# Kernel optimization log

Measured on AMD Instinct MI355X. Metric: run time of the kernel, lower is better.

The kernel has to match this reference:

```python
import jax, jax.numpy as jnp
import numpy as np

OUT_F, IN_F = 8192, 8192
RATIO = 0.05


def setup_inputs() -> dict:
    rng = np.random.default_rng(0)
    # Simulate the quantization performed in OrthoLinear.__init__ with numpy.
    w = (rng.standard_normal((OUT_F, IN_F)) * 0.02).astype(np.float32)
    w_abs = np.abs(w)
    k_idx = min(int(IN_F * 0.995), IN_F - 1)
    # torch.kthvalue(k) = k-th smallest (1-indexed) -> partition index k-1
    robust_max = np.partition(w_abs, k_idx - 1, axis=1)[:, k_idx - 1][:, None]
    robust_max = np.maximum(robust_max, 1e-6)
    scales = (robust_max / 7.0).astype(np.float32)
    w_int = np.clip(np.round(w / scales), -7, 7).astype(np.float32)
    resid = w - w_int * scales
    # top-k |residual| entries form the sparse CSR correction
    k = max(int(resid.size * RATIO), 1)
    metric = np.abs(resid).ravel()
    idx = np.argpartition(metric, -k)[-k:]
    idx.sort()
    rows = idx // IN_F
    cols = (idx % IN_F).astype(np.int32)
    vals = resid.ravel()[idx].astype(np.float16)
    ptr = np.zeros(OUT_F + 1, np.int32)
    ptr[1:] = np.cumsum(np.bincount(rows, minlength=OUT_F)).astype(np.int32)
    # pack two int4 (offset by +8) per byte: even cols -> low nibble, odd -> high
    offs = (w_int + 8.0).astype(np.uint8)
    packed = (offs[:, 0::2] | (offs[:, 1::2] << 4)).astype(np.int32)
    x = jax.random.normal(jax.random.key(0), (4, 8, IN_F), jnp.float32)
    return {
        "x": x,
        "base_packed": jnp.asarray(packed),
        "scales": jnp.asarray(scales.reshape(-1)),
        "ortho_vals": jnp.asarray(vals),
        "ortho_indices": jnp.asarray(cols),
        "ortho_ptr": jnp.asarray(ptr),
        "alpha": jnp.float32(1.0),
    }


def reference(x, base_packed, scales, ortho_vals, ortho_indices, ortho_ptr, alpha):
    lead = x.shape[:-1]
    in_f = x.shape[-1]
    out_f = base_packed.shape[0]
    xf = x.reshape(-1, in_f).astype(jnp.float32)  # [N, in]
    # dequantize packed int4 base weight: interleave low/high nibbles
    low = base_packed & 0xF
    high = (base_packed >> 4) & 0xF
    w_int = jnp.stack([low, high], axis=-1).reshape(out_f, in_f).astype(jnp.float32) - 8.0
    w_base = w_int * scales[:, None]  # [out, in]
    # CSR residual -> scatter into dense [out, in] (disjoint coords), then GEMM
    nnz = ortho_vals.shape[0]
    row_ids = jnp.searchsorted(ortho_ptr, jnp.arange(nnz, dtype=jnp.int32), side="right") - 1
    w_res = jnp.zeros((out_f, in_f), jnp.float32).at[row_ids, ortho_indices].add(
        ortho_vals.astype(jnp.float32)
    )
    out = xf @ w_base.T + alpha * (xf @ w_res.T)  # [N, out]
    return out.reshape(lead + (out_f,))
```

## Files before the change

kernel.cpp:

```cpp
#include <hip/hip_runtime.h>


#define IN_F 8192
#define OUT_F 8192
#define NROW 32
#define KSPLIT 8
#define KSEG (IN_F / KSPLIT)
#define CHUNKS (KSEG / 32)
#define SLICE (NROW * OUT_F)

typedef __attribute__((ext_vector_type(8))) short short8v;
typedef __attribute__((ext_vector_type(4))) float f32x4;

union Frag {
  int4 v;
  unsigned int u[4];
  short8v s;
};

__device__ __forceinline__ unsigned int cvt_pk_bf16(float lo, float hi) {
  unsigned int r;
  asm("v_cvt_pk_bf16_f32 %0, %1, %2" : "=v"(r) : "v"(lo), "v"(hi));
  return r;
}

__device__ __forceinline__ unsigned short f2bf(float f) {
  unsigned int u = __float_as_uint(f);
  u += 0x7FFFu + ((u >> 16) & 1u);
  return (unsigned short)(u >> 16);
}

__global__ __launch_bounds__(256) void prep_kernel(
    const float* __restrict__ x, unsigned short* __restrict__ x_hi,
    unsigned short* __restrict__ x_lo, unsigned short* __restrict__ xTb) {
  __shared__ unsigned short T[64 * 33];
  int tid = threadIdx.x;
  int k0 = blockIdx.x * 64;
  int kk = tid & 63;
  int ng = tid >> 6;
#pragma unroll
  for (int p = 0; p < 8; ++p) {
    int n = p * 4 + ng;
    int idx = n * IN_F + k0 + kk;
    float v = x[idx];
    unsigned short h = f2bf(v);
    float hf = __uint_as_float((unsigned int)h << 16);
    unsigned short l = f2bf(v - hf);
    x_hi[idx] = h;
    x_lo[idx] = l;
    T[kk * 33 + n] = h;
  }
  __syncthreads();
  int kr = tid >> 2, q = tid & 3;
  unsigned int s0 = T[kr * 33 + q * 8 + 0], s1 = T[kr * 33 + q * 8 + 1];
  unsigned int s2 = T[kr * 33 + q * 8 + 2], s3 = T[kr * 33 + q * 8 + 3];
  unsigned int s4 = T[kr * 33 + q * 8 + 4], s5 = T[kr * 33 + q * 8 + 5];
  unsigned int s6 = T[kr * 33 + q * 8 + 6], s7 = T[kr * 33 + q * 8 + 7];
  int4 wv;
  wv.x = (int)(s0 | (s1 << 16));
  wv.y = (int)(s2 | (s3 << 16));
  wv.z = (int)(s4 | (s5 << 16));
  wv.w = (int)(s6 | (s7 << 16));
  ((int4*)xTb)[(size_t)(k0 + kr) * 4 + q] = wv;
}

__global__ __launch_bounds__(256, 4) void dense_kernel(
    const int* __restrict__ packed, const float* __restrict__ scales,
    const unsigned short* __restrict__ x_hi,
    const unsigned short* __restrict__ x_lo, float* __restrict__ part) {
  int tid = threadIdx.x;
  int lane = tid & 63;
  int w = tid >> 6;
  int og = blockIdx.x >> 3;
  int g = blockIdx.x & 7;
  int lo16 = lane & 15;
  int lhi = lane >> 4;

  int o = og * 64 + w * 16 + lo16;
  int kbeg = g * KSEG;
  const int4* wp = (const int4*)(packed + (size_t)o * (IN_F / 2) + (kbeg >> 1)) + lhi;
  const unsigned short* xh = x_hi + lo16 * IN_F + kbeg + 8 * lhi;
  const unsigned short* xl = x_lo + lo16 * IN_F + kbeg + 8 * lhi;

  f32x4 acc0 = {0.f, 0.f, 0.f, 0.f};
  f32x4 acc1 = {0.f, 0.f, 0.f, 0.f};

  Frag wA, h0A, l0A, h1A, l1A;
  Frag wB, h0B, l0B, h1B, l1B;

#define LOADIN(W_, H0, L0, H1, L1, c)                  \
  W_.v = wp[(c) * 4];                                  \
  H0.v = *(const int4*)(xh + (c) * 32);                \
  L0.v = *(const int4*)(xl + (c) * 32);                \
  H1.v = *(const int4*)(xh + 16 * IN_F + (c) * 32);    \
  L1.v = *(const int4*)(xl + 16 * IN_F + (c) * 32);

#define COMPUTE(W_, H0, L0, H1, L1)                                               \
  {                                                                               \
    Frag b;                                                                       \
    b.u[0] = cvt_pk_bf16((float)(W_.v.x & 15) - 8.0f, (float)(W_.v.x >> 4) - 8.0f); \
    b.u[1] = cvt_pk_bf16((float)(W_.v.y & 15) - 8.0f, (float)(W_.v.y >> 4) - 8.0f); \
    b.u[2] = cvt_pk_bf16((float)(W_.v.z & 15) - 8.0f, (float)(W_.v.z >> 4) - 8.0f); \
    b.u[3] = cvt_pk_bf16((float)(W_.v.w & 15) - 8.0f, (float)(W_.v.w >> 4) - 8.0f); \
    acc0 = __builtin_amdgcn_mfma_f32_16x16x32_bf16(H0.s, b.s, acc0, 0, 0, 0);     \
    acc0 = __builtin_amdgcn_mfma_f32_16x16x32_bf16(L0.s, b.s, acc0, 0, 0, 0);     \
    acc1 = __builtin_amdgcn_mfma_f32_16x16x32_bf16(H1.s, b.s, acc1, 0, 0, 0);     \
    acc1 = __builtin_amdgcn_mfma_f32_16x16x32_bf16(L1.s, b.s, acc1, 0, 0, 0);     \
  }

  LOADIN(wA, h0A, l0A, h1A, l1A, 0)
  for (int c = 0; c < CHUNKS; c += 2) {
    LOADIN(wB, h0B, l0B, h1B, l1B, c + 1)
    COMPUTE(wA, h0A, l0A, h1A, l1A)
    if (c + 2 < CHUNKS) {
      LOADIN(wA, h0A, l0A, h1A, l1A, c + 2)
    }
    COMPUTE(wB, h0B, l0B, h1B, l1B)
  }
#undef LOADIN
#undef COMPUTE

  float sc = scales[o];
  float* ps = part + (size_t)g * SLICE;
#pragma unroll
  for (int r = 0; r < 4; ++r) {
    int m = lhi * 4 + r;
    ps[(size_t)m * OUT_F + o] = sc * acc0[r];
    ps[(size_t)(m + 16) * OUT_F + o] = sc * acc1[r];
  }
}

__global__ __launch_bounds__(256) void sparse_kernel(
    const float* __restrict__ vals, const int* __restrict__ cols,
    const int* __restrict__ rptr, const float* __restrict__ alphap,
    const unsigned short* __restrict__ xTb, float* __restrict__ part8) {
  __shared__ float red[4][64 * 33];
  int tid = threadIdx.x;
  int lane = tid & 63;
  int w = tid >> 6;
  float alpha = alphap[0];
  float* R = red[w];
#pragma unroll 1
  for (int rr = 0; rr < 2; ++rr) {
    int ro = blockIdx.x * 8 + w * 2 + rr;
    int js = rptr[ro], je = rptr[ro + 1];
    float acc[32];
#pragma unroll
    for (int i = 0; i < 32; ++i) acc[i] = 0.f;

    int j = js + lane;
    float vc = 0.f;
    int cc = 0;
    if (j < je) { vc = vals[j]; cc = cols[j]; }
    while (j < je) {
      int jn = j + 64;
      float vn = 0.f;
      int cn = 0;
      if (jn < je) { vn = vals[jn]; cn = cols[jn]; }
      const int4* xp = (const int4*)(xTb + (size_t)cc * NROW);
      int4 q0 = xp[0], q1 = xp[1], q2 = xp[2], q3 = xp[3];
#define UNP(dw, base)                                                          \
  {                                                                            \
    unsigned int ud = (unsigned int)(dw);                                      \
    acc[base] = fmaf(vc, __uint_as_float(ud << 16), acc[base]);                \
    acc[base + 1] = fmaf(vc, __uint_as_float(ud & 0xFFFF0000u), acc[base + 1]); \
  }
      UNP(q0.x, 0) UNP(q0.y, 2) UNP(q0.z, 4) UNP(q0.w, 6)
      UNP(q1.x, 8) UNP(q1.y, 10) UNP(q1.z, 12) UNP(q1.w, 14)
      UNP(q2.x, 16) UNP(q2.y, 18) UNP(q2.z, 20) UNP(q2.w, 22)
      UNP(q3.x, 24) UNP(q3.y, 26) UNP(q3.z, 28) UNP(q3.w, 30)
#undef UNP
      j = jn;
      vc = vn;
      cc = cn;
    }
#pragma unroll
    for (int i = 0; i < 32; ++i) R[lane * 33 + i] = acc[i];
    int cidx = lane & 31;
    int h = lane >> 5;
    float sum = 0.f;
#pragma unroll
    for (int r2 = 0; r2 < 32; ++r2) sum += R[(h * 32 + r2) * 33 + cidx];
    sum += __shfl_xor(sum, 32, 64);
    if (lane < 32) part8[(size_t)lane * OUT_F + ro] = alpha * sum;
  }
}

__global__ __launch_bounds__(256) void reduce_kernel(
    const float* __restrict__ part, float* __restrict__ out) {
  int i = blockIdx.x * 256 + threadIdx.x;
  const float4* p4 = (const float4*)part;
  float4 s = p4[i];
#pragma unroll
  for (int sl = 1; sl < 9; ++sl) {
    float4 t = p4[i + sl * (SLICE / 4)];
    s.x += t.x; s.y += t.y; s.z += t.z; s.w += t.w;
  }
  ((float4*)out)[i] = s;
}

extern "C" void kernel_launch(void* const* d_in, const int* in_sizes, int n_in,
                              void* d_out, int out_size, void* d_ws, size_t ws_size,
                              hipStream_t stream) {
  const float* x = (const float*)d_in[0];
  const int* packed = (const int*)d_in[1];
  const float* scales = (const float*)d_in[2];
  const float* vals = (const float*)d_in[3];
  const int* cols = (const int*)d_in[4];
  const int* rptr = (const int*)d_in[5];
  const float* alphap = (const float*)d_in[6];
  float* out = (float*)d_out;

  unsigned short* x_hi = (unsigned short*)d_ws;
  unsigned short* x_lo = x_hi + NROW * IN_F;
  unsigned short* xTb = x_lo + NROW * IN_F;
  float* part = (float*)(xTb + NROW * IN_F);

  prep_kernel<<<IN_F / 64, 256, 0, stream>>>(x, x_hi, x_lo, xTb);
  dense_kernel<<<(OUT_F / 64) * KSPLIT, 256, 0, stream>>>(
      packed, scales, x_hi, x_lo, part);
  sparse_kernel<<<OUT_F / 8, 256, 0, stream>>>(
      vals, cols, rptr, alphap, xTb, part + (size_t)8 * SLICE);
  reduce_kernel<<<(SLICE / 4) / 256, 256, 0, stream>>>(part, out);
}
```

Baseline: 305.3 us.

## Stage dense-kernel tiles into swizzled LDS via async global_load_lds double buffering

The dense int4 GEMM kernel now copies packed weights and the bf16 hi/lo activations into a double-buffered, XOR-swizzled shared-memory tile with direct global-to-LDS loads, instead of each lane loading its fragments straight from global memory. Each stage covers 64 K-elements and is overlapped with MFMA compute on the other buffer, synchronised with vmcnt waits and barriers. The goal is coalesced global traffic and better latency hiding. In exchange it adds two barriers per step, about 32 KB of LDS per block, and drops the occupancy hint from launch bounds, which may lower waves per CU.

```diff
diff --git a/kernel.cpp b/kernel.cpp
--- a/kernel.cpp
+++ b/kernel.cpp
@@ -6,7 +6,11 @@
 #define NROW 32
 #define KSPLIT 8
 #define KSEG (IN_F / KSPLIT)
-#define CHUNKS (KSEG / 32)
+#define KS 64
+#define NSTEP (KSEG / KS)
+#define PK_TILE 8192
+#define X_TILE 4096
+#define BUF_SZ (PK_TILE + 2 * X_TILE)
 #define SLICE (NROW * OUT_F)
 
 typedef __attribute__((ext_vector_type(8))) short short8v;
@@ -64,10 +68,11 @@
   ((int4*)xTb)[(size_t)(k0 + kr) * 4 + q] = wv;
 }
 
-__global__ __launch_bounds__(256, 4) void dense_kernel(
+__global__ __launch_bounds__(256) void dense_kernel(
     const int* __restrict__ packed, const float* __restrict__ scales,
     const unsigned short* __restrict__ x_hi,
     const unsigned short* __restrict__ x_lo, float* __restrict__ part) {
+  __shared__ char lds[2][BUF_SZ];
   int tid = threadIdx.x;
   int lane = tid & 63;
   int w = tid >> 6;
@@ -76,50 +81,75 @@
   int lo16 = lane & 15;
   int lhi = lane >> 4;
 
-  int o = og * 64 + w * 16 + lo16;
-  int kbeg = g * KSEG;
-  const int4* wp = (const int4*)(packed + (size_t)o * (IN_F / 2) + (kbeg >> 1)) + lhi;
-  const unsigned short* xh = x_hi + lo16 * IN_F + kbeg + 8 * lhi;
-  const unsigned short* xl = x_lo + lo16 * IN_F + kbeg + 8 * lhi;
+  int L0 = tid * 16;
+  int pr0 = L0 >> 7;
+  int pb0 = (L0 & 127) ^ ((pr0 & 7) << 4);
+  const char* pkB = (const char*)packed;
+  const char* psrc0 = pkB + (size_t)(og * 64 + pr0) * 16384 + g * 2048 + pb0;
+  const char* psrc1 = pkB + (size_t)(og * 64 + pr0 + 32) * 16384 + g * 2048 + pb0;
+  int xr = tid >> 3;
+  int xb = ((tid & 7) * 16) ^ ((xr & 7) << 4);
+  const char* xhsrc = (const char*)x_hi + (size_t)xr * (IN_F * 2) + g * 2048 + xb;
+  const char* xlsrc = (const char*)x_lo + (size_t)xr * (IN_F * 2) + g * 2048 + xb;
+  int woff = w * 1024;
+
+#define STAGE(s, b)                                                          \
+  {                                                                          \
+    int so_ = (s) * 128;                                                     \
+    __builtin_amdgcn_global_load_lds((const unsigned int*)(psrc0 + so_),     \
+        (unsigned int*)(&lds[b][0] + woff), 16, 0, 0);                       \
+    __builtin_amdgcn_global_load_lds((const unsigned int*)(psrc1 + so_),     \
+        (unsigned int*)(&lds[b][4096] + woff), 16, 0, 0);                    \
+    __builtin_amdgcn_global_load_lds((const unsigned int*)(xhsrc + so_),     \
+        (unsigned int*)(&lds[b][PK_TILE] + woff), 16, 0, 0);                 \
+    __builtin_amdgcn_global_load_lds((const unsigned int*)(xlsrc + so_),     \
+        (unsigned int*)(&lds[b][PK_TILE + X_TILE] + woff), 16, 0, 0);        \
+  }
 
   f32x4 acc0 = {0.f, 0.f, 0.f, 0.f};
   f32x4 acc1 = {0.f, 0.f, 0.f, 0.f};
-
-  Frag wA, h0A, l0A, h1A, l1A;
-  Frag wB, h0B, l0B, h1B, l1B;
-
-#define LOADIN(W_, H0, L0, H1, L1, c)                  \
-  W_.v = wp[(c) * 4];                                  \
-  H0.v = *(const int4*)(xh + (c) * 32);                \
-  L0.v = *(const int4*)(xl + (c) * 32);                \
-  H1.v = *(const int4*)(xh + 16 * IN_F + (c) * 32);    \
-  L1.v = *(const int4*)(xl + 16 * IN_F + (c) * 32);
-
-#define COMPUTE(W_, H0, L0, H1, L1)                                               \
-  {                                                                               \
-    Frag b;                                                                       \
-    b.u[0] = cvt_pk_bf16((float)(W_.v.x & 15) - 8.0f, (float)(W_.v.x >> 4) - 8.0f); \
-    b.u[1] = cvt_pk_bf16((float)(W_.v.y & 15) - 8.0f, (float)(W_.v.y >> 4) - 8.0f); \
-    b.u[2] = cvt_pk_bf16((float)(W_.v.z & 15) - 8.0f, (float)(W_.v.z >> 4) - 8.0f); \
-    b.u[3] = cvt_pk_bf16((float)(W_.v.w & 15) - 8.0f, (float)(W_.v.w >> 4) - 8.0f); \
-    acc0 = __builtin_amdgcn_mfma_f32_16x16x32_bf16(H0.s, b.s, acc0, 0, 0, 0);     \
-    acc0 = __builtin_amdgcn_mfma_f32_16x16x32_bf16(L0.s, b.s, acc0, 0, 0, 0);     \
-    acc1 = __builtin_amdgcn_mfma_f32_16x16x32_bf16(H1.s, b.s, acc1, 0, 0, 0);     \
-    acc1 = __builtin_amdgcn_mfma_f32_16x16x32_bf16(L1.s, b.s, acc1, 0, 0, 0);     \
-  }
-
-  LOADIN(wA, h0A, l0A, h1A, l1A, 0)
-  for (int c = 0; c < CHUNKS; c += 2) {
-    LOADIN(wB, h0B, l0B, h1B, l1B, c + 1)
-    COMPUTE(wA, h0A, l0A, h1A, l1A)
-    if (c + 2 < CHUNKS) {
-      LOADIN(wA, h0A, l0A, h1A, l1A, c + 2)
+  int prow = w * 16 + lo16;
+  int pswz = (prow & 7) << 4;
+  int xswz = (lo16 & 7) << 4;
+
+#define COMPCHUNK(b, cp)                                                      \
+  {                                                                           \
+    int pby = (cp) * 64 + 16 * lhi;                                           \
+    Frag bb, a0h, a0l, a1h, a1l;                                              \
+    bb.v = *(const int4*)&lds[b][prow * 128 + (pby ^ pswz)];                  \
+    a0h.v = *(const int4*)&lds[b][PK_TILE + lo16 * 128 + (pby ^ xswz)];       \
+    a0l.v = *(const int4*)&lds[b][PK_TILE + X_TILE + lo16 * 128 + (pby ^ xswz)]; \
+    a1h.v = *(const int4*)&lds[b][PK_TILE + (lo16 + 16) * 128 + (pby ^ xswz)];   \
+    a1l.v = *(const int4*)&lds[b][PK_TILE + X_TILE + (lo16 + 16) * 128 + (pby ^ xswz)]; \
+    Frag bf;                                                                  \
+    bf.u[0] = cvt_pk_bf16((float)(bb.v.x & 15) - 8.0f, (float)(bb.v.x >> 4) - 8.0f); \
+    bf.u[1] = cvt_pk_bf16((float)(bb.v.y & 15) - 8.0f, (float)(bb.v.y >> 4) - 8.0f); \
+    bf.u[2] = cvt_pk_bf16((float)(bb.v.z & 15) - 8.0f, (float)(bb.v.z >> 4) - 8.0f); \
+    bf.u[3] = cvt_pk_bf16((float)(bb.v.w & 15) - 8.0f, (float)(bb.v.w >> 4) - 8.0f); \
+    acc0 = __builtin_amdgcn_mfma_f32_16x16x32_bf16(a0h.s, bf.s, acc0, 0, 0, 0); \
+    acc0 = __builtin_amdgcn_mfma_f32_16x16x32_bf16(a0l.s, bf.s, acc0, 0, 0, 0); \
+    acc1 = __builtin_amdgcn_mfma_f32_16x16x32_bf16(a1h.s, bf.s, acc1, 0, 0, 0); \
+    acc1 = __builtin_amdgcn_mfma_f32_16x16x32_bf16(a1l.s, bf.s, acc1, 0, 0, 0); \
+  }
+
+  STAGE(0, 0)
+  for (int s = 0; s < NSTEP; ++s) {
+    int b = s & 1;
+    if (s + 1 < NSTEP) {
+      STAGE(s + 1, (s + 1) & 1)
+      asm volatile("s_waitcnt vmcnt(4)" ::: "memory");
+    } else {
+      asm volatile("s_waitcnt vmcnt(0)" ::: "memory");
     }
-    COMPUTE(wB, h0B, l0B, h1B, l1B)
-  }
-#undef LOADIN
-#undef COMPUTE
-
+    __syncthreads();
+    COMPCHUNK(b, 0)
+    COMPCHUNK(b, 1)
+    __syncthreads();
+  }
+#undef STAGE
+#undef COMPCHUNK
+
+  int o = og * 64 + w * 16 + lo16;
   float sc = scales[o];
   float* ps = part + (size_t)g * SLICE;
 #pragma unroll
```

After: 263.8 us. 1.16x faster.
